# Performance work log

Measured on AMD Instinct MI355X. Metric: run time of the kernel, lower is better.

The kernel has to match this reference:

```python
import jax, jax.numpy as jnp
import numpy as np

B, H, K = 4096, 256, 16
INPUT_DIM, XPRIME_DIM = 8, 64
D = INPUT_DIM * XPRIME_DIM  # 512
LN_EPS = 1e-5


def setup_inputs() -> dict:
    key = jax.random.key(0)
    ks = jax.random.split(key, 12)
    s1 = 1.0  # Linear(1, D): fan_in=1
    sD = 1.0 / np.sqrt(D)
    sH = 1.0 / np.sqrt(H)
    return {
        "h_prev_rnn": jax.random.normal(ks[0], (B, H), jnp.float32),
        "x_l": jax.random.normal(ks[1], (B, INPUT_DIM), jnp.float32),
        "x_ext": jax.random.normal(ks[2], (B, K), jnp.float32),
        # stacked per-expert MetaNet params
        "meta_w1": jax.random.uniform(ks[3], (K, D), jnp.float32, -s1, s1),
        "meta_b1": jax.random.uniform(ks[4], (K, D), jnp.float32, -s1, s1),
        "meta_w2": jax.random.uniform(ks[5], (K, D, D), jnp.float32, -sD, sD),
        "meta_b2": jax.random.uniform(ks[6], (K, D), jnp.float32, -sD, sD),
        # gating net
        "gw1": jax.random.uniform(ks[7], (H, H), jnp.float32, -sH, sH),
        "gb1": jax.random.uniform(ks[8], (H,), jnp.float32, -sH, sH),
        "gw2": jax.random.uniform(ks[9], (H, K), jnp.float32, -sH, sH),
        "gb2": jax.random.uniform(ks[10], (K,), jnp.float32, -sH, sH),
        # LayerNorm([input_dim, xprime_dim]) affine params
        "ln_g": jnp.ones((INPUT_DIM, XPRIME_DIM), jnp.float32),
        "ln_b": jnp.zeros((INPUT_DIM, XPRIME_DIM), jnp.float32),
        "theta0": jnp.zeros((1, INPUT_DIM, XPRIME_DIM), jnp.float32),
    }


def reference(h_prev_rnn, x_l, x_ext, meta_w1, meta_b1, meta_w2, meta_b2,
              gw1, gb1, gw2, gb2, ln_g, ln_b, theta0):
    # MetaNet layer1 (Linear(1, D)): scalar input per expert -> [B, K, D]
    h1 = jnp.tanh(x_ext[:, :, None] * meta_w1[None] + meta_b1[None])
    # MetaNet layer2: per-expert DxD GEMM
    h2 = jnp.tanh(jnp.einsum('bkd,kde->bke', h1, meta_w2) + meta_b2[None])
    W = h2.reshape(h2.shape[0], K, INPUT_DIM, XPRIME_DIM)  # [B,K,i,e]
    # LayerNorm over last two dims jointly, affine
    mu = W.mean(axis=(-2, -1), keepdims=True)
    var = W.var(axis=(-2, -1), keepdims=True)
    W = (W - mu) * jax.lax.rsqrt(var + LN_EPS) * ln_g + ln_b
    # gating: softmax over experts (epoch/top_k = None path)
    logits = jnp.tanh(h_prev_rnn @ gw1 + gb1) @ gw2 + gb2
    gates = jax.nn.softmax(logits, axis=-1)  # [B, K]
    theta = jnp.einsum('bk,bkie->bie', gates, W) + theta0  # [B, i, e]
    x_prime = jnp.einsum('bi,bie->be', x_l, theta)  # [B, e]
    return (x_prime, theta)
```

## Files before the change

kernel.cpp:

```cpp
#include <hip/hip_runtime.h>
#include <stdint.h>

#define NB 4096
#define NH 256
#define NK 16
#define ND 512
#define NC 48
#define NM 48
#define RCHEB 7.0f
#define PI_F 3.14159265358979323846f

typedef _Float16 f16;
using half8   = __attribute__((ext_vector_type(8))) _Float16;
using float4v = __attribute__((ext_vector_type(4))) float;

__device__ __forceinline__ float fast_tanh(float x) {
  float e = __builtin_amdgcn_exp2f(x * 2.88539008177793f);
  return 1.0f - 2.0f * __builtin_amdgcn_rcpf(e + 1.0f);
}

__global__ __launch_bounds__(256) void k_gates(
    const float* __restrict__ h_prev,
    const float* __restrict__ gw1, const float* __restrict__ gb1,
    const float* __restrict__ gw2, const float* __restrict__ gb2,
    float* __restrict__ gates) {
  __shared__ float sbuf[4096];
  const int t = threadIdx.x;
  const int b0 = blockIdx.x * 8;
  float* sh_h = sbuf;
  float* sh_t = sbuf + 2048;
  for (int r = 0; r < 8; ++r) sh_h[r * 256 + t] = h_prev[(b0 + r) * NH + t];
  __syncthreads();
  float acc[8];
  const float bias = gb1[t];
#pragma unroll
  for (int r = 0; r < 8; ++r) acc[r] = bias;
  for (int i = 0; i < NH; i += 4) {
    const float w0 = gw1[(i + 0) * NH + t];
    const float w1v = gw1[(i + 1) * NH + t];
    const float w2v = gw1[(i + 2) * NH + t];
    const float w3 = gw1[(i + 3) * NH + t];
#pragma unroll
    for (int r = 0; r < 8; ++r) {
      const float4 hv = *(const float4*)&sh_h[r * 256 + i];
      acc[r] += hv.x * w0 + hv.y * w1v + hv.z * w2v + hv.w * w3;
    }
  }
#pragma unroll
  for (int r = 0; r < 8; ++r) sh_t[t * 8 + r] = fast_tanh(acc[r]);
  __syncthreads();
  if (t < 128) {
    const int r = t >> 4, k = t & 15;
    float lg = gb2[k];
    for (int j = 0; j < NH; ++j) lg += sh_t[j * 8 + r] * gw2[j * NK + k];
    float m = lg;
    for (int off = 1; off < 16; off <<= 1) m = fmaxf(m, __shfl_xor(m, off, 16));
    const float e = __builtin_amdgcn_exp2f((lg - m) * 1.44269504f);
    float s = e;
    for (int off = 1; off < 16; off <<= 1) s += __shfl_xor(s, off, 16);
    gates[(b0 + r) * NK + k] = e * __builtin_amdgcn_rcpf(s);
  }
}

__global__ __launch_bounds__(256) void k_stanh(
    const float* __restrict__ w1, const float* __restrict__ b1,
    float* __restrict__ Sg, float* __restrict__ ctg) {
  const int t = threadIdx.x;
  const int k = blockIdx.x >> 3;
  const int d0 = (blockIdx.x & 7) * 64;
  if (blockIdx.x == 0) {
    for (int i = t; i < NM * NC; i += 256) {
      const int m = i / 48, j = i - m * 48;
      const int r = (j * (2 * m + 1)) % 192;
      const float fac = (j == 0 ? 1.0f : 2.0f) * (1.0f / 48.0f);
      ctg[i] = cosf(PI_F * (float)r * (1.0f / 96.0f)) * fac;
    }
  }
  const int dl = t >> 2, mg = t & 3;
  const int d = d0 + dl;
  const float a = w1[k * ND + d];
  const float b = b1[k * ND + d];
  float o[12];
#pragma unroll
  for (int mi = 0; mi < 12; ++mi) {
    const int m = mg * 12 + mi;
    const float cx = cosf(PI_F * (float)(2 * m + 1) * (1.0f / 96.0f));
    o[mi] = fast_tanh(fmaf(a, RCHEB * cx, b));
  }
  float* dst = Sg + ((size_t)k * ND + d) * NM + mg * 12;
  *(float4*)&dst[0] = *(float4*)&o[0];
  *(float4*)&dst[4] = *(float4*)&o[4];
  *(float4*)&dst[8] = *(float4*)&o[8];
}

__global__ __launch_bounds__(256) void k_coef(
    const float* __restrict__ w2, const float* __restrict__ Sg,
    const float* __restrict__ ctg, float* __restrict__ Cc0,
    float* __restrict__ Cc1) {
  __shared__ __align__(16) char smem[34848];
  float (*w2s)[68] = (float(*)[68])smem;
  float (*Gl)[68]  = (float(*)[68])smem;
  const int t = threadIdx.x;
  const int blk = blockIdx.x;
  const int k = blk >> 4;
  const int e0 = ((blk >> 1) & 7) * 64;
  const int dh = blk & 1;
  const int el = t & 63;
  const int mqu = __builtin_amdgcn_readfirstlane(t >> 6);

  const float* w2k = w2 + (size_t)k * ND * ND + e0;
  float g[12];
#pragma unroll
  for (int i = 0; i < 12; ++i) g[i] = 0.f;

  float4 ld[8];
#pragma unroll
  for (int it = 0; it < 8; ++it) {
    const int idx = t + it * 256;
    const int d = idx >> 4, f4 = idx & 15;
    ld[it] = *(const float4*)&w2k[(size_t)(dh * 256 + d) * ND + f4 * 4];
  }

  for (int cc = 0; cc < 2; ++cc) {
    const int c = 2 * dh + cc;
#pragma unroll
    for (int it = 0; it < 8; ++it) {
      const int idx = t + it * 256;
      const int d = idx >> 4, f4 = idx & 15;
      *(float4*)&w2s[d][f4 * 4] = ld[it];
    }
    __syncthreads();
    if (cc == 0) {
#pragma unroll
      for (int it = 0; it < 8; ++it) {
        const int idx = t + it * 256;
        const int d = idx >> 4, f4 = idx & 15;
        ld[it] = *(const float4*)&w2k[(size_t)(dh * 256 + 128 + d) * ND + f4 * 4];
      }
    }
    const float* Sp = Sg + ((size_t)k * ND + c * 128) * NM + mqu * 12;
#pragma unroll 4
    for (int d = 0; d < 128; ++d) {
      const float wv = w2s[d][el];
      const float4 s0 = *(const float4*)&Sp[d * NM];
      const float4 s1 = *(const float4*)&Sp[d * NM + 4];
      const float4 s2 = *(const float4*)&Sp[d * NM + 8];
      g[0] = fmaf(s0.x, wv, g[0]);
      g[1] = fmaf(s0.y, wv, g[1]);
      g[2] = fmaf(s0.z, wv, g[2]);
      g[3] = fmaf(s0.w, wv, g[3]);
      g[4] = fmaf(s1.x, wv, g[4]);
      g[5] = fmaf(s1.y, wv, g[5]);
      g[6] = fmaf(s1.z, wv, g[6]);
      g[7] = fmaf(s1.w, wv, g[7]);
      g[8] = fmaf(s2.x, wv, g[8]);
      g[9] = fmaf(s2.y, wv, g[9]);
      g[10] = fmaf(s2.z, wv, g[10]);
      g[11] = fmaf(s2.w, wv, g[11]);
    }
    __syncthreads();
  }

#pragma unroll
  for (int mi = 0; mi < 12; ++mi) Gl[mqu * 12 + mi][el] = g[mi];
  __syncthreads();

  float cacc[12];
#pragma unroll
  for (int i = 0; i < 12; ++i) cacc[i] = 0.f;
#pragma unroll 4
  for (int m = 0; m < NM; ++m) {
    const float gv = Gl[m][el];
    const float4 c0 = *(const float4*)&ctg[m * 48 + mqu * 12];
    const float4 c1 = *(const float4*)&ctg[m * 48 + mqu * 12 + 4];
    const float4 c2 = *(const float4*)&ctg[m * 48 + mqu * 12 + 8];
    cacc[0] = fmaf(c0.x, gv, cacc[0]);
    cacc[1] = fmaf(c0.y, gv, cacc[1]);
    cacc[2] = fmaf(c0.z, gv, cacc[2]);
    cacc[3] = fmaf(c0.w, gv, cacc[3]);
    cacc[4] = fmaf(c1.x, gv, cacc[4]);
    cacc[5] = fmaf(c1.y, gv, cacc[5]);
    cacc[6] = fmaf(c1.z, gv, cacc[6]);
    cacc[7] = fmaf(c1.w, gv, cacc[7]);
    cacc[8] = fmaf(c2.x, gv, cacc[8]);
    cacc[9] = fmaf(c2.y, gv, cacc[9]);
    cacc[10] = fmaf(c2.z, gv, cacc[10]);
    cacc[11] = fmaf(c2.w, gv, cacc[11]);
  }
  float* Cc = dh ? Cc1 : Cc0;
#pragma unroll
  for (int jj = 0; jj < 12; ++jj) {
    const int j = mqu * 12 + jj;
    Cc[((size_t)(k * 2 + (j >> 5)) * ND + e0 + el) * 32 + (j & 31)] = cacc[jj];
  }
}

__global__ __launch_bounds__(256) void k_pack(
    const float* __restrict__ Cc0, const float* __restrict__ Cc1,
    const float* __restrict__ b2, f16* __restrict__ Cbf) {
  const int idx = blockIdx.x * 256 + threadIdx.x;
  const int flat8 = idx * 8;
  const int k2 = flat8 >> 14;
  const int rem = flat8 & 16383;
  const int e = rem >> 5, o8 = rem & 31;
  const int j0 = (k2 & 1) * 32 + o8;
  f16 o[8];
  if (j0 >= 48) {
#pragma unroll
    for (int i = 0; i < 8; ++i) o[i] = (f16)0.f;
  } else {
    float v[8];
    *(float4*)&v[0] = *(const float4*)&Cc0[flat8];
    *(float4*)&v[4] = *(const float4*)&Cc0[flat8 + 4];
    const float4 u0 = *(const float4*)&Cc1[flat8];
    const float4 u1 = *(const float4*)&Cc1[flat8 + 4];
    v[0] += u0.x; v[1] += u0.y; v[2] += u0.z; v[3] += u0.w;
    v[4] += u1.x; v[5] += u1.y; v[6] += u1.z; v[7] += u1.w;
    if (((k2 & 1) == 0) && (o8 == 0)) v[0] += b2[(k2 >> 1) * ND + e];
#pragma unroll
    for (int i = 0; i < 8; ++i) o[i] = (f16)v[i];
  }
  *(uint4*)&Cbf[flat8] = *(uint4*)o;
}

__global__ __launch_bounds__(256) void k_eval(
    const f16* __restrict__ Cbf, const float* __restrict__ gates,
    const float* __restrict__ x_ext, const float* __restrict__ x_l,
    const float* __restrict__ ln_g, const float* __restrict__ ln_b,
    const float* __restrict__ theta0, float* __restrict__ out) {
  __shared__ __align__(16) char sm[47616];
  f16* Tlds = (f16*)sm;
  float (*xp)[16][68] = (float(*)[16][68])sm;
  float (*lnbuf)[16][4][2] = (float(*)[16][4][2])(sm + 36864);
  float (*sx)[16] = (float(*)[16])(sm + 45056);
  float (*sg)[16] = (float(*)[16])(sm + 46080);
  float (*sxl)[8] = (float(*)[8])(sm + 47104);
  const int t = threadIdx.x;
  const int l = t & 63, wn = t >> 6;
  const int q = l >> 4, m16 = l & 15;
  const int b0 = blockIdx.x * 16;

  const f16* Bbase = Cbf + ((size_t)(wn * 128 + m16)) * 32 + q * 8;
  half8 BrA[16], BrB[16];
  auto loadB = [&](int k, half8(&dst)[16]) {
#pragma unroll
    for (int bni = 0; bni < 8; ++bni) {
      dst[bni * 2 + 0] =
          *(const half8*)(Bbase + ((size_t)(k * 2 + 0) * ND + bni * 16) * 32);
      dst[bni * 2 + 1] =
          *(const half8*)(Bbase + ((size_t)(k * 2 + 1) * ND + bni * 16) * 32);
    }
  };
  loadB(0, BrA);

  {
    const int row = t >> 4, kk = t & 15;
    sx[row][kk] = x_ext[(b0 + row) * NK + kk];
    sg[row][kk] = gates[(b0 + row) * NK + kk];
    if (t < 128) sxl[t >> 3][t & 7] = x_l[(b0 + (t >> 3)) * 8 + (t & 7)];
  }
  __syncthreads();

  {
    const int k = t >> 4, row = t & 15;
    f16* T0 = &Tlds[(2 * k) * 576 + row * 36];
    f16* T1 = &Tlds[(2 * k + 1) * 576 + row * 36];
    float u = sx[row][k] * (1.0f / RCHEB);
    u = fminf(1.0f, fmaxf(-1.0f, u));
    const float u2 = u + u;
    float tp = 1.0f, tc = u;
    T0[0] = (f16)1.0f;
    T0[1] = (f16)u;
#pragma unroll
    for (int j = 2; j < 48; ++j) {
      const float tn = fmaf(u2, tc, -tp);
      tp = tc; tc = tn;
      if (j < 32) T0[j] = (f16)tn; else T1[j - 32] = (f16)tn;
    }
#pragma unroll
    for (int j = 48; j < 64; ++j) T1[j - 32] = (f16)0.f;
  }
  __syncthreads();

  float lng[8], lnb[8];
#pragma unroll
  for (int bni = 0; bni < 8; ++bni) {
    const int col = wn * 128 + bni * 16 + m16;
    lng[bni] = ln_g[col];
    lnb[bni] = ln_b[col];
  }

  float th[8][4];
#pragma unroll
  for (int bni = 0; bni < 8; ++bni)
#pragma unroll
    for (int rr = 0; rr < 4; ++rr) th[bni][rr] = 0.f;

  const f16* Abase = Tlds + m16 * 36 + q * 8;
  const float4v z = {0.f, 0.f, 0.f, 0.f};

  auto stepA = [&](int k, const half8(&Br)[16], float4v(&acc)[8],
                   float(&s)[4], float(&s2)[4]) {
    const half8 a0 = *(const half8*)(Abase + (2 * k) * 576);
    const half8 a1 = *(const half8*)(Abase + (2 * k + 1) * 576);
#pragma unroll
    for (int bni = 0; bni < 8; ++bni) {
      acc[bni] = __builtin_amdgcn_mfma_f32_16x16x32_f16(a0, Br[2 * bni], z, 0, 0, 0);
      acc[bni] = __builtin_amdgcn_mfma_f32_16x16x32_f16(a1, Br[2 * bni + 1],
                                                        acc[bni], 0, 0, 0);
    }
#pragma unroll
    for (int rr = 0; rr < 4; ++rr) { s[rr] = 0.f; s2[rr] = 0.f; }
#pragma unroll
    for (int bni = 0; bni < 8; ++bni)
#pragma unroll
      for (int rr = 0; rr < 4; ++rr) {
        const float v = fast_tanh(acc[bni][rr]);
        acc[bni][rr] = v;
        s[rr] += v;
        s2[rr] = fmaf(v, v, s2[rr]);
      }
#pragma unroll
    for (int off = 1; off < 16; off <<= 1)
#pragma unroll
      for (int rr = 0; rr < 4; ++rr) {
        s[rr] += __shfl_xor(s[rr], off, 64);
        s2[rr] += __shfl_xor(s2[rr], off, 64);
      }
  };
  auto lnwrite = [&](int k, const float(&s)[4], const float(&s2)[4]) {
    if (m16 == 0) {
#pragma unroll
      for (int rr = 0; rr < 4; ++rr) {
        lnbuf[k][q * 4 + rr][wn][0] = s[rr];
        lnbuf[k][q * 4 + rr][wn][1] = s2[rr];
      }
    }
  };
  auto apply = [&](int k, const float4v(&acc)[8]) {
#pragma unroll
    for (int rr = 0; rr < 4; ++rr) {
      const int row = q * 4 + rr;
      const float4 pa = *(const float4*)&lnbuf[k][row][0][0];
      const float4 pb = *(const float4*)&lnbuf[k][row][2][0];
      const float S1 = pa.x + pa.z + pb.x + pb.z;
      const float S2 = pa.y + pa.w + pb.y + pb.w;
      const float mu = S1 * (1.0f / 512.0f);
      const float var = fmaf(S2, 1.0f / 512.0f, -mu * mu);
      const float rs = __builtin_amdgcn_rsqf(var + 1e-5f);
      const float gate = sg[row][k];
      const float a = gate * rs;
#pragma unroll
      for (int bni = 0; bni < 8; ++bni)
        th[bni][rr] = fmaf(a * lng[bni], acc[bni][rr] - mu,
                           fmaf(gate, lnb[bni], th[bni][rr]));
    }
  };

  float sA[4], s2A[4], sB[4], s2B[4];
  float4v accA[8], accB[8];

  stepA(0, BrA, accA, sA, s2A);
  lnwrite(0, sA, s2A);
  loadB(1, BrB);
  __syncthreads();
  for (int kp = 0; kp < 7; ++kp) {
    stepA(2 * kp + 1, BrB, accB, sB, s2B);
    apply(2 * kp, accA);
    lnwrite(2 * kp + 1, sB, s2B);
    loadB(2 * kp + 2, BrA);
    __syncthreads();
    stepA(2 * kp + 2, BrA, accA, sA, s2A);
    apply(2 * kp + 1, accB);
    lnwrite(2 * kp + 2, sA, s2A);
    loadB(2 * kp + 3, BrB);
    __syncthreads();
  }
  stepA(15, BrB, accB, sB, s2B);
  apply(14, accA);
  lnwrite(15, sB, s2B);
  __syncthreads();
  apply(15, accB);

  float* thbase = out + (size_t)NB * 64;
#pragma unroll
  for (int bni = 0; bni < 8; ++bni) {
    const int col = wn * 128 + bni * 16 + m16;
    const float t0v = theta0[col];
#pragma unroll
    for (int rr = 0; rr < 4; ++rr) {
      const float o = th[bni][rr] + t0v;
      th[bni][rr] = o;
      thbase[(size_t)(b0 + q * 4 + rr) * ND + col] = o;
    }
  }
#pragma unroll
  for (int rr = 0; rr < 4; ++rr) {
    const int row = q * 4 + rr;
    const float xlA = sxl[row][2 * wn], xlB = sxl[row][2 * wn + 1];
#pragma unroll
    for (int g4 = 0; g4 < 4; ++g4)
      xp[wn][row][g4 * 16 + m16] = xlA * th[g4][rr] + xlB * th[g4 + 4][rr];
  }
  __syncthreads();
  {
    const int row = t >> 4, ec = (t & 15) * 4;
    const float4 p0 = *(const float4*)&xp[0][row][ec];
    const float4 p1 = *(const float4*)&xp[1][row][ec];
    const float4 p2 = *(const float4*)&xp[2][row][ec];
    const float4 p3 = *(const float4*)&xp[3][row][ec];
    float4 r;
    r.x = p0.x + p1.x + p2.x + p3.x;
    r.y = p0.y + p1.y + p2.y + p3.y;
    r.z = p0.z + p1.z + p2.z + p3.z;
    r.w = p0.w + p1.w + p2.w + p3.w;
    *(float4*)&out[(size_t)(b0 + row) * 64 + ec] = r;
  }
}

extern "C" void kernel_launch(void* const* d_in, const int* in_sizes, int n_in,
                              void* d_out, int out_size, void* d_ws, size_t ws_size,
                              hipStream_t stream) {
  const float* h_prev = (const float*)d_in[0];
  const float* x_l    = (const float*)d_in[1];
  const float* x_ext  = (const float*)d_in[2];
  const float* mw1    = (const float*)d_in[3];
  const float* mb1    = (const float*)d_in[4];
  const float* mw2    = (const float*)d_in[5];
  const float* mb2    = (const float*)d_in[6];
  const float* gw1    = (const float*)d_in[7];
  const float* gb1    = (const float*)d_in[8];
  const float* gw2    = (const float*)d_in[9];
  const float* gb2    = (const float*)d_in[10];
  const float* ln_g   = (const float*)d_in[11];
  const float* ln_b   = (const float*)d_in[12];
  const float* th0    = (const float*)d_in[13];
  float* out = (float*)d_out;

  char* ws = (char*)d_ws;
  float* gates = (float*)ws;
  f16* Cbf     = (f16*)(ws + 0x40000);
  float* Cc0   = (float*)(ws + 0x140000);
  float* Cc1   = (float*)(ws + 0x340000);
  float* Sg    = (float*)(ws + 0x540000);
  float* ctg   = (float*)(ws + 0x740000);

  hipLaunchKernelGGL(k_gates, dim3(512), dim3(256), 0, stream,
                     h_prev, gw1, gb1, gw2, gb2, gates);
  hipLaunchKernelGGL(k_stanh, dim3(128), dim3(256), 0, stream,
                     mw1, mb1, Sg, ctg);
  hipLaunchKernelGGL(k_coef, dim3(256), dim3(256), 0, stream,
                     mw2, Sg, ctg, Cc0, Cc1);
  hipLaunchKernelGGL(k_pack, dim3(256), dim3(256), 0, stream,
                     Cc0, Cc1, mb2, Cbf);
  hipLaunchKernelGGL(k_eval, dim3(256), dim3(256), 0, stream,
                     Cbf, gates, x_ext, x_l, ln_g, ln_b, th0, out);
}
```

Before: 194.1 us.

## Merge gating and Chebyshev sampling kernels; split coef and eval grids finer

Folds the tanh-sampling kernel into the gating kernel as extra blocks, which removes one launch. The coefficient kernel now splits the D reduction four ways with no LDS staging of w2 and writes four partials that k_pack sums. The eval kernel handles 8 batch rows per block instead of 16, doubling the grid to 512 blocks. Half of each eval block's lanes now idle in the MFMA tiles (rows padded with zeros), and the partial buffers add extra global traffic.

Result: faster. 186.0 us (-4.1%).

```diff
diff --git a/kernel.cpp b/kernel.cpp
--- a/kernel.cpp
+++ b/kernel.cpp
@@ -9,6 +9,7 @@
 #define NM 48
 #define RCHEB 7.0f
 #define PI_F 3.14159265358979323846f
+#define CCPART (NK * 2 * ND * 32)
 
 typedef _Float16 f16;
 using half8   = __attribute__((ext_vector_type(8))) _Float16;
@@ -19,14 +20,47 @@
   return 1.0f - 2.0f * __builtin_amdgcn_rcpf(e + 1.0f);
 }
 
-__global__ __launch_bounds__(256) void k_gates(
+__global__ __launch_bounds__(256) void k_gs(
     const float* __restrict__ h_prev,
     const float* __restrict__ gw1, const float* __restrict__ gb1,
     const float* __restrict__ gw2, const float* __restrict__ gb2,
-    float* __restrict__ gates) {
+    const float* __restrict__ w1, const float* __restrict__ b1,
+    float* __restrict__ gates, float* __restrict__ Sg, float* __restrict__ ctg) {
   __shared__ float sbuf[4096];
   const int t = threadIdx.x;
-  const int b0 = blockIdx.x * 8;
+  const int blk = blockIdx.x;
+
+  if (blk >= 512) {
+    const int sb = blk - 512;
+    const int k = sb >> 3;
+    const int d0 = (sb & 7) * 64;
+    if (sb == 0) {
+      for (int i = t; i < NM * NC; i += 256) {
+        const int m = i / 48, j = i - m * 48;
+        const int r = (j * (2 * m + 1)) % 192;
+        const float fac = (j == 0 ? 1.0f : 2.0f) * (1.0f / 48.0f);
+        ctg[i] = cosf(PI_F * (float)r * (1.0f / 96.0f)) * fac;
+      }
+    }
+    const int dl = t >> 2, mg = t & 3;
+    const int d = d0 + dl;
+    const float a = w1[k * ND + d];
+    const float b = b1[k * ND + d];
+    float o[12];
+#pragma unroll
+    for (int mi = 0; mi < 12; ++mi) {
+      const int m = mg * 12 + mi;
+      const float cx = cosf(PI_F * (float)(2 * m + 1) * (1.0f / 96.0f));
+      o[mi] = fast_tanh(fmaf(a, RCHEB * cx, b));
+    }
+    float* dst = Sg + ((size_t)k * ND + d) * NM + mg * 12;
+    *(float4*)&dst[0] = *(float4*)&o[0];
+    *(float4*)&dst[4] = *(float4*)&o[4];
+    *(float4*)&dst[8] = *(float4*)&o[8];
+    return;
+  }
+
+  const int b0 = blk * 8;
   float* sh_h = sbuf;
   float* sh_t = sbuf + 2048;
   for (int r = 0; r < 8; ++r) sh_h[r * 256 + t] = h_prev[(b0 + r) * NH + t];
@@ -62,103 +96,42 @@
   }
 }
 
-__global__ __launch_bounds__(256) void k_stanh(
-    const float* __restrict__ w1, const float* __restrict__ b1,
-    float* __restrict__ Sg, float* __restrict__ ctg) {
-  const int t = threadIdx.x;
-  const int k = blockIdx.x >> 3;
-  const int d0 = (blockIdx.x & 7) * 64;
-  if (blockIdx.x == 0) {
-    for (int i = t; i < NM * NC; i += 256) {
-      const int m = i / 48, j = i - m * 48;
-      const int r = (j * (2 * m + 1)) % 192;
-      const float fac = (j == 0 ? 1.0f : 2.0f) * (1.0f / 48.0f);
-      ctg[i] = cosf(PI_F * (float)r * (1.0f / 96.0f)) * fac;
-    }
-  }
-  const int dl = t >> 2, mg = t & 3;
-  const int d = d0 + dl;
-  const float a = w1[k * ND + d];
-  const float b = b1[k * ND + d];
-  float o[12];
-#pragma unroll
-  for (int mi = 0; mi < 12; ++mi) {
-    const int m = mg * 12 + mi;
-    const float cx = cosf(PI_F * (float)(2 * m + 1) * (1.0f / 96.0f));
-    o[mi] = fast_tanh(fmaf(a, RCHEB * cx, b));
-  }
-  float* dst = Sg + ((size_t)k * ND + d) * NM + mg * 12;
-  *(float4*)&dst[0] = *(float4*)&o[0];
-  *(float4*)&dst[4] = *(float4*)&o[4];
-  *(float4*)&dst[8] = *(float4*)&o[8];
-}
-
 __global__ __launch_bounds__(256) void k_coef(
     const float* __restrict__ w2, const float* __restrict__ Sg,
-    const float* __restrict__ ctg, float* __restrict__ Cc0,
-    float* __restrict__ Cc1) {
-  __shared__ __align__(16) char smem[34848];
-  float (*w2s)[68] = (float(*)[68])smem;
-  float (*Gl)[68]  = (float(*)[68])smem;
+    const float* __restrict__ ctg, float* __restrict__ Cc) {
+  __shared__ float Gl[48][68];
   const int t = threadIdx.x;
   const int blk = blockIdx.x;
-  const int k = blk >> 4;
-  const int e0 = ((blk >> 1) & 7) * 64;
-  const int dh = blk & 1;
+  const int k = blk >> 5;
+  const int e0 = ((blk >> 2) & 7) * 64;
+  const int dq = blk & 3;
   const int el = t & 63;
   const int mqu = __builtin_amdgcn_readfirstlane(t >> 6);
 
-  const float* w2k = w2 + (size_t)k * ND * ND + e0;
+  const float* w2p = w2 + ((size_t)k * ND + dq * 128) * ND + e0 + el;
+  const float* Sp = Sg + ((size_t)k * ND + dq * 128) * NM + mqu * 12;
+
   float g[12];
 #pragma unroll
   for (int i = 0; i < 12; ++i) g[i] = 0.f;
-
-  float4 ld[8];
-#pragma unroll
-  for (int it = 0; it < 8; ++it) {
-    const int idx = t + it * 256;
-    const int d = idx >> 4, f4 = idx & 15;
-    ld[it] = *(const float4*)&w2k[(size_t)(dh * 256 + d) * ND + f4 * 4];
-  }
-
-  for (int cc = 0; cc < 2; ++cc) {
-    const int c = 2 * dh + cc;
-#pragma unroll
-    for (int it = 0; it < 8; ++it) {
-      const int idx = t + it * 256;
-      const int d = idx >> 4, f4 = idx & 15;
-      *(float4*)&w2s[d][f4 * 4] = ld[it];
-    }
-    __syncthreads();
-    if (cc == 0) {
-#pragma unroll
-      for (int it = 0; it < 8; ++it) {
-        const int idx = t + it * 256;
-        const int d = idx >> 4, f4 = idx & 15;
-        ld[it] = *(const float4*)&w2k[(size_t)(dh * 256 + 128 + d) * ND + f4 * 4];
-      }
-    }
-    const float* Sp = Sg + ((size_t)k * ND + c * 128) * NM + mqu * 12;
 #pragma unroll 4
-    for (int d = 0; d < 128; ++d) {
-      const float wv = w2s[d][el];
-      const float4 s0 = *(const float4*)&Sp[d * NM];
-      const float4 s1 = *(const float4*)&Sp[d * NM + 4];
-      const float4 s2 = *(const float4*)&Sp[d * NM + 8];
-      g[0] = fmaf(s0.x, wv, g[0]);
-      g[1] = fmaf(s0.y, wv, g[1]);
-      g[2] = fmaf(s0.z, wv, g[2]);
-      g[3] = fmaf(s0.w, wv, g[3]);
-      g[4] = fmaf(s1.x, wv, g[4]);
-      g[5] = fmaf(s1.y, wv, g[5]);
-      g[6] = fmaf(s1.z, wv, g[6]);
-      g[7] = fmaf(s1.w, wv, g[7]);
-      g[8] = fmaf(s2.x, wv, g[8]);
-      g[9] = fmaf(s2.y, wv, g[9]);
-      g[10] = fmaf(s2.z, wv, g[10]);
-      g[11] = fmaf(s2.w, wv, g[11]);
-    }
-    __syncthreads();
+  for (int d = 0; d < 128; ++d) {
+    const float wv = w2p[(size_t)d * ND];
+    const float4 s0 = *(const float4*)&Sp[d * NM];
+    const float4 s1 = *(const float4*)&Sp[d * NM + 4];
+    const float4 s2 = *(const float4*)&Sp[d * NM + 8];
+    g[0] = fmaf(s0.x, wv, g[0]);
+    g[1] = fmaf(s0.y, wv, g[1]);
+    g[2] = fmaf(s0.z, wv, g[2]);
+    g[3] = fmaf(s0.w, wv, g[3]);
+    g[4] = fmaf(s1.x, wv, g[4]);
+    g[5] = fmaf(s1.y, wv, g[5]);
+    g[6] = fmaf(s1.z, wv, g[6]);
+    g[7] = fmaf(s1.w, wv, g[7]);
+    g[8] = fmaf(s2.x, wv, g[8]);
+    g[9] = fmaf(s2.y, wv, g[9]);
+    g[10] = fmaf(s2.z, wv, g[10]);
+    g[11] = fmaf(s2.w, wv, g[11]);
   }
 
 #pragma unroll
@@ -187,17 +160,17 @@
     cacc[10] = fmaf(c2.z, gv, cacc[10]);
     cacc[11] = fmaf(c2.w, gv, cacc[11]);
   }
-  float* Cc = dh ? Cc1 : Cc0;
+  float* Ccq = Cc + (size_t)dq * CCPART;
 #pragma unroll
   for (int jj = 0; jj < 12; ++jj) {
     const int j = mqu * 12 + jj;
-    Cc[((size_t)(k * 2 + (j >> 5)) * ND + e0 + el) * 32 + (j & 31)] = cacc[jj];
+    Ccq[((size_t)(k * 2 + (j >> 5)) * ND + e0 + el) * 32 + (j & 31)] = cacc[jj];
   }
 }
 
 __global__ __launch_bounds__(256) void k_pack(
-    const float* __restrict__ Cc0, const float* __restrict__ Cc1,
-    const float* __restrict__ b2, f16* __restrict__ Cbf) {
+    const float* __restrict__ Cc, const float* __restrict__ b2,
+    f16* __restrict__ Cbf) {
   const int idx = blockIdx.x * 256 + threadIdx.x;
   const int flat8 = idx * 8;
   const int k2 = flat8 >> 14;
@@ -210,12 +183,15 @@
     for (int i = 0; i < 8; ++i) o[i] = (f16)0.f;
   } else {
     float v[8];
-    *(float4*)&v[0] = *(const float4*)&Cc0[flat8];
-    *(float4*)&v[4] = *(const float4*)&Cc0[flat8 + 4];
-    const float4 u0 = *(const float4*)&Cc1[flat8];
-    const float4 u1 = *(const float4*)&Cc1[flat8 + 4];
-    v[0] += u0.x; v[1] += u0.y; v[2] += u0.z; v[3] += u0.w;
-    v[4] += u1.x; v[5] += u1.y; v[6] += u1.z; v[7] += u1.w;
+#pragma unroll
+    for (int i = 0; i < 8; ++i) v[i] = 0.f;
+#pragma unroll
+    for (int p = 0; p < 4; ++p) {
+      const float4 u0 = *(const float4*)&Cc[(size_t)p * CCPART + flat8];
+      const float4 u1 = *(const float4*)&Cc[(size_t)p * CCPART + flat8 + 4];
+      v[0] += u0.x; v[1] += u0.y; v[2] += u0.z; v[3] += u0.w;
+      v[4] += u1.x; v[5] += u1.y; v[6] += u1.z; v[7] += u1.w;
+    }
     if (((k2 & 1) == 0) && (o8 == 0)) v[0] += b2[(k2 >> 1) * ND + e];
 #pragma unroll
     for (int i = 0; i < 8; ++i) o[i] = (f16)v[i];
@@ -228,17 +204,17 @@
     const float* __restrict__ x_ext, const float* __restrict__ x_l,
     const float* __restrict__ ln_g, const float* __restrict__ ln_b,
     const float* __restrict__ theta0, float* __restrict__ out) {
-  __shared__ __align__(16) char sm[47616];
+  __shared__ __align__(16) char sm[43264];
   f16* Tlds = (f16*)sm;
-  float (*xp)[16][68] = (float(*)[16][68])sm;
-  float (*lnbuf)[16][4][2] = (float(*)[16][4][2])(sm + 36864);
-  float (*sx)[16] = (float(*)[16])(sm + 45056);
-  float (*sg)[16] = (float(*)[16])(sm + 46080);
-  float (*sxl)[8] = (float(*)[8])(sm + 47104);
+  float (*xp)[8][68] = (float(*)[8][68])sm;
+  float (*lnbuf)[8][4][2] = (float(*)[8][4][2])(sm + 36864);
+  float (*sx)[16] = (float(*)[16])(sm + 40960);
+  float (*sg)[16] = (float(*)[16])(sm + 41472);
+  float (*sxl)[8] = (float(*)[8])(sm + 41984);
   const int t = threadIdx.x;
   const int l = t & 63, wn = t >> 6;
   const int q = l >> 4, m16 = l & 15;
-  const int b0 = blockIdx.x * 16;
+  const int b0 = blockIdx.x * 8;
 
   const f16* Bbase = Cbf + ((size_t)(wn * 128 + m16)) * 32 + q * 8;
   half8 BrA[16], BrB[16];
@@ -253,19 +229,21 @@
   };
   loadB(0, BrA);
 
-  {
+  if (t < 128) {
     const int row = t >> 4, kk = t & 15;
     sx[row][kk] = x_ext[(b0 + row) * NK + kk];
     sg[row][kk] = gates[(b0 + row) * NK + kk];
-    if (t < 128) sxl[t >> 3][t & 7] = x_l[(b0 + (t >> 3)) * 8 + (t & 7)];
-  }
-  __syncthreads();
-
-  {
-    const int k = t >> 4, row = t & 15;
-    f16* T0 = &Tlds[(2 * k) * 576 + row * 36];
-    f16* T1 = &Tlds[(2 * k + 1) * 576 + row * 36];
-    float u = sx[row][k] * (1.0f / RCHEB);
+  } else if (t < 192) {
+    const int tt = t - 128;
+    sxl[tt >> 3][tt & 7] = x_l[(b0 + (tt >> 3)) * 8 + (tt & 7)];
+  }
+  __syncthreads();
+
+  if (t < 128) {
+    const int kk = t >> 3, row = t & 7;
+    f16* T0 = &Tlds[(2 * kk) * 576 + row * 36];
+    f16* T1 = &Tlds[(2 * kk + 1) * 576 + row * 36];
+    float u = sx[row][kk] * (1.0f / RCHEB);
     u = fminf(1.0f, fmaxf(-1.0f, u));
     const float u2 = u + u;
     float tp = 1.0f, tc = u;
@@ -279,6 +257,12 @@
     }
 #pragma unroll
     for (int j = 48; j < 64; ++j) T1[j - 32] = (f16)0.f;
+  } else {
+    const int tt = t - 128;
+    const int ksub = tt >> 2;
+    f16* Z = &Tlds[ksub * 576 + (8 + (tt & 3) * 2) * 36];
+#pragma unroll
+    for (int j = 0; j < 72; ++j) Z[j] = (f16)0.f;
   }
   __syncthreads();
 
@@ -329,7 +313,7 @@
       }
   };
   auto lnwrite = [&](int k, const float(&s)[4], const float(&s2)[4]) {
-    if (m16 == 0) {
+    if (m16 == 0 && q < 2) {
 #pragma unroll
       for (int rr = 0; rr < 4; ++rr) {
         lnbuf[k][q * 4 + rr][wn][0] = s[rr];
@@ -338,22 +322,24 @@
     }
   };
   auto apply = [&](int k, const float4v(&acc)[8]) {
-#pragma unroll
-    for (int rr = 0; rr < 4; ++rr) {
-      const int row = q * 4 + rr;
-      const float4 pa = *(const float4*)&lnbuf[k][row][0][0];
-      const float4 pb = *(const float4*)&lnbuf[k][row][2][0];
-      const float S1 = pa.x + pa.z + pb.x + pb.z;
-      const float S2 = pa.y + pa.w + pb.y + pb.w;
-      const float mu = S1 * (1.0f / 512.0f);
-      const float var = fmaf(S2, 1.0f / 512.0f, -mu * mu);
-      const float rs = __builtin_amdgcn_rsqf(var + 1e-5f);
-      const float gate = sg[row][k];
-      const float a = gate * rs;
-#pragma unroll
-      for (int bni = 0; bni < 8; ++bni)
-        th[bni][rr] = fmaf(a * lng[bni], acc[bni][rr] - mu,
-                           fmaf(gate, lnb[bni], th[bni][rr]));
+    if (q < 2) {
+#pragma unroll
+      for (int rr = 0; rr < 4; ++rr) {
+        const int row = q * 4 + rr;
+        const float4 pa = *(const float4*)&lnbuf[k][row][0][0];
+        const float4 pb = *(const float4*)&lnbuf[k][row][2][0];
+        const float S1 = pa.x + pa.z + pb.x + pb.z;
+        const float S2 = pa.y + pa.w + pb.y + pb.w;
+        const float mu = S1 * (1.0f / 512.0f);
+        const float var = fmaf(S2, 1.0f / 512.0f, -mu * mu);
+        const float rs = __builtin_amdgcn_rsqf(var + 1e-5f);
+        const float gate = sg[row][k];
+        const float a = gate * rs;
+#pragma unroll
+        for (int bni = 0; bni < 8; ++bni)
+          th[bni][rr] = fmaf(a * lng[bni], acc[bni][rr] - mu,
+                             fmaf(gate, lnb[bni], th[bni][rr]));
+      }
     }
   };
 
@@ -383,38 +369,39 @@
   apply(15, accB);
 
   float* thbase = out + (size_t)NB * 64;
-#pragma unroll
-  for (int bni = 0; bni < 8; ++bni) {
-    const int col = wn * 128 + bni * 16 + m16;
-    const float t0v = theta0[col];
+  if (q < 2) {
+#pragma unroll
+    for (int bni = 0; bni < 8; ++bni) {
+      const int col = wn * 128 + bni * 16 + m16;
+      const float t0v = theta0[col];
+#pragma unroll
+      for (int rr = 0; rr < 4; ++rr) {
+        const float o = th[bni][rr] + t0v;
+        th[bni][rr] = o;
+        thbase[(size_t)(b0 + q * 4 + rr) * ND + col] = o;
+      }
+    }
 #pragma unroll
     for (int rr = 0; rr < 4; ++rr) {
-      const float o = th[bni][rr] + t0v;
-      th[bni][rr] = o;
-      thbase[(size_t)(b0 + q * 4 + rr) * ND + col] = o;
-    }
-  }
-#pragma unroll
-  for (int rr = 0; rr < 4; ++rr) {
-    const int row = q * 4 + rr;
-    const float xlA = sxl[row][2 * wn], xlB = sxl[row][2 * wn + 1];
-#pragma unroll
-    for (int g4 = 0; g4 < 4; ++g4)
-      xp[wn][row][g4 * 16 + m16] = xlA * th[g4][rr] + xlB * th[g4 + 4][rr];
+      const int row = q * 4 + rr;
+      const float xlA = sxl[row][2 * wn], xlB = sxl[row][2 * wn + 1];
+#pragma unroll
+      for (int g4 = 0; g4 < 4; ++g4)
+        xp[wn][row][g4 * 16 + m16] = xlA * th[g4][rr] + xlB * th[g4 + 4][rr];
+    }
   }
   __syncthreads();
   {
-    const int row = t >> 4, ec = (t & 15) * 4;
-    const float4 p0 = *(const float4*)&xp[0][row][ec];
-    const float4 p1 = *(const float4*)&xp[1][row][ec];
-    const float4 p2 = *(const float4*)&xp[2][row][ec];
-    const float4 p3 = *(const float4*)&xp[3][row][ec];
-    float4 r;
-    r.x = p0.x + p1.x + p2.x + p3.x;
-    r.y = p0.y + p1.y + p2.y + p3.y;
-    r.z = p0.z + p1.z + p2.z + p3.z;
-    r.w = p0.w + p1.w + p2.w + p3.w;
-    *(float4*)&out[(size_t)(b0 + row) * 64 + ec] = r;
+    const int idx = t * 2;
+    const int row = idx >> 6, ec = idx & 63;
+    float2 r = {0.f, 0.f};
+#pragma unroll
+    for (int w4 = 0; w4 < 4; ++w4) {
+      const float2 p = *(const float2*)&xp[w4][row][ec];
+      r.x += p.x;
+      r.y += p.y;
+    }
+    *(float2*)&out[(size_t)(b0 + row) * 64 + ec] = r;
   }
 }
 
@@ -440,19 +427,16 @@
   char* ws = (char*)d_ws;
   float* gates = (float*)ws;
   f16* Cbf     = (f16*)(ws + 0x40000);
-  float* Cc0   = (float*)(ws + 0x140000);
-  float* Cc1   = (float*)(ws + 0x340000);
-  float* Sg    = (float*)(ws + 0x540000);
-  float* ctg   = (float*)(ws + 0x740000);
-
-  hipLaunchKernelGGL(k_gates, dim3(512), dim3(256), 0, stream,
-                     h_prev, gw1, gb1, gw2, gb2, gates);
-  hipLaunchKernelGGL(k_stanh, dim3(128), dim3(256), 0, stream,
-                     mw1, mb1, Sg, ctg);
-  hipLaunchKernelGGL(k_coef, dim3(256), dim3(256), 0, stream,
-                     mw2, Sg, ctg, Cc0, Cc1);
+  float* Cc    = (float*)(ws + 0x140000);
+  float* Sg    = (float*)(ws + 0x940000);
+  float* ctg   = (float*)(ws + 0xB00000);
+
+  hipLaunchKernelGGL(k_gs, dim3(640), dim3(256), 0, stream,
+                     h_prev, gw1, gb1, gw2, gb2, mw1, mb1, gates, Sg, ctg);
+  hipLaunchKernelGGL(k_coef, dim3(512), dim3(256), 0, stream,
+                     mw2, Sg, ctg, Cc);
   hipLaunchKernelGGL(k_pack, dim3(256), dim3(256), 0, stream,
-                     Cc0, Cc1, mb2, Cbf);
-  hipLaunchKernelGGL(k_eval, dim3(256), dim3(256), 0, stream,
+                     Cc, mb2, Cbf);
+  hipLaunchKernelGGL(k_eval, dim3(512), dim3(256), 0, stream,
                      Cbf, gates, x_ext, x_l, ln_g, ln_b, th0, out);
 }
```
